# Kernel tuning notes

Hardware: AMD Instinct MI355X
Metric: run time of the kernel (lower is better)

Reference implementation:

```python
import jax, jax.numpy as jnp
import numpy as np
from jax.scipy.special import logsumexp

B, N, D = 8, 2048, 256
X_SLIDE, Y_SLIDE = 0.05, 0.05
ITERS = 20  # self.sinkhorn_iterations


def setup_inputs() -> dict:
    key = jax.random.key(0)
    k1, k2 = jax.random.split(key)
    return {
        "node_features": jax.random.normal(k1, (B, D, N), dtype=jnp.float32),
        "node_positions": jax.random.uniform(k2, (B, N, 2), dtype=jnp.float32),
        "active_nodes": jnp.ones((B, N), dtype=bool),
        "alpha": jnp.ones((1,), dtype=jnp.float32),  # bin_score parameter
    }


def log_sinkhorn_iterations(Z, log_mu, log_nu, iters):
    """Log-space Sinkhorn. Z: (b, M, K); log_mu: (b, M); log_nu: (b, K)."""
    u0 = jnp.zeros_like(log_mu)
    v0 = jnp.zeros_like(log_nu)

    def body(carry, _):
        u, v = carry
        u = log_mu - logsumexp(Z + v[:, None, :], axis=2)
        v = log_nu - logsumexp(Z + u[:, :, None], axis=1)
        return (u, v), None

    (u, v), _ = jax.lax.scan(body, (u0, v0), None, length=iters)
    return Z + u[:, :, None] + v[:, None, :]


def log_optimal_transport(scores, alpha, iters):
    """scores: (b, m, n); alpha: scalar bin score."""
    b, m, n = scores.shape
    dt = scores.dtype
    ms = jnp.asarray(m, dt)
    ns = jnp.asarray(n, dt)
    bins0 = jnp.broadcast_to(alpha, (b, m, 1))
    bins1 = jnp.broadcast_to(alpha, (b, 1, n))
    corner = jnp.broadcast_to(alpha, (b, 1, 1))
    couplings = jnp.concatenate(
        [jnp.concatenate([scores, bins0], axis=2),
         jnp.concatenate([bins1, corner], axis=2)], axis=1)  # (b, m+1, n+1)
    norm = -jnp.log(ms + ns)
    log_mu = jnp.concatenate([jnp.broadcast_to(norm, (m,)), (jnp.log(ns) + norm)[None]])
    log_nu = jnp.concatenate([jnp.broadcast_to(norm, (n,)), (jnp.log(ms) + norm)[None]])
    log_mu = jnp.broadcast_to(log_mu[None], (b, m + 1))
    log_nu = jnp.broadcast_to(log_nu[None], (b, n + 1))
    Z = log_sinkhorn_iterations(couplings, log_mu, log_nu, iters)
    return Z - norm


def spatial_cost(positions, x_slide, y_slide):
    """positions: (N, 2) -> bool (N, N) adjacency; diagonal excluded via 1e6 fill."""
    y = positions[:, 0]
    x = positions[:, 1]
    yd = jnp.abs(y[:, None] - y[None, :])
    xd = jnp.abs(x[:, None] - x[None, :])
    eye = jnp.eye(positions.shape[0], dtype=bool)
    yd = jnp.where(eye, 1e6, yd)
    xd = jnp.where(eye, 1e6, xd)
    return (xd <= x_slide * 2.0) & (yd <= y_slide * 2.0)


def reference(node_features, node_positions, active_nodes, alpha):
    # all nodes active -> indexing by active_nodes is identity, vectorize over batch
    a = alpha.reshape(())
    d = node_features.shape[1]
    scale = jnp.asarray(d, node_features.dtype) ** 0.5
    scores = jnp.einsum('bdn,bdm->bnm', node_features, node_features) / scale  # (B, N, N)
    n = scores.shape[-1]
    eye = jnp.eye(n, dtype=bool)
    scores = jnp.where(eye[None], -jnp.inf, scores)  # fill_diagonal_(-inf)
    Z = log_optimal_transport(scores, a, ITERS)  # (B, N+1, N+1)
    S = jnp.exp(Z)
    cost = jax.vmap(lambda p: spatial_cost(p, X_SLIDE, Y_SLIDE))(node_positions)
    S = S.at[:, :-1, :-1].multiply(cost.astype(S.dtype))
    return S
```

## Files before the change

kernel.cpp:

```cpp
#include <hip/hip_runtime.h>
#include <math.h>

#define BN    8
#define NN    2048
#define NP1   2049
#define VSTR  2056
#define DD    256
#define NITER 20
#define NBLK  256
#define GRP   32

typedef float f32x2 __attribute__((ext_vector_type(2)));
typedef float f32x4_t __attribute__((ext_vector_type(4)));
typedef short short8 __attribute__((ext_vector_type(8)));


__global__ void init_kernel(float* __restrict__ bvec, int nb, float* __restrict__ sums,
                            int* __restrict__ bar) {
    int tid = blockIdx.x * blockDim.x + threadIdx.x;
    int stride = gridDim.x * blockDim.x;
    for (int i = tid; i < nb; i += stride) bvec[i] = 1.0f;
    for (int i = tid; i < 41 * BN; i += stride) sums[i] = (i < BN) ? (float)NN : 0.0f;
    if (tid < BN * GRP) bar[tid] = 0;
}

__device__ __forceinline__ unsigned short f2bf(float f) {
    unsigned u = __builtin_bit_cast(unsigned, f);
    return (unsigned short)((u + 0x7fffu + ((u >> 16) & 1u)) >> 16);
}

__global__ __launch_bounds__(256) void f_to_bf16(const float* __restrict__ F,
                                                 unsigned char* __restrict__ F16) {
    int x0 = blockIdx.x * 64, k0 = blockIdx.y * 64, bb = blockIdx.z;
    __shared__ unsigned short tile[64][68];
    int t = threadIdx.x;
    const float* Fb = F + (size_t)bb * DD * NN;
#pragma unroll
    for (int q = 0; q < 16; q++) {
        int idx = q * 256 + t;
        int kk = idx >> 6, xx = idx & 63;
        tile[xx][kk] = f2bf(Fb[(size_t)(k0 + kk) * NN + x0 + xx]);
    }
    __syncthreads();
    int r = t >> 2, c = t & 3;
    const unsigned long long* src = (const unsigned long long*)&tile[r][c * 16];
    unsigned long long v0 = src[0], v1 = src[1], v2 = src[2], v3 = src[3];
    unsigned char* dst = F16 + (((size_t)bb * NN + x0 + r) * DD + k0) * 2 + c * 32;
    ((unsigned long long*)dst)[0] = v0;
    ((unsigned long long*)dst)[1] = v1;
    ((unsigned long long*)dst)[2] = v2;
    ((unsigned long long*)dst)[3] = v3;
}

__global__ __launch_bounds__(256) void build_k3(const unsigned char* __restrict__ F16,
                                                unsigned char* __restrict__ K8) {
    int idx = blockIdx.x, ti = 0;
    while (idx >= 16 - ti) { idx -= 16 - ti; ti++; }
    int tj = ti + idx;
    int bb = blockIdx.z;
    int i0 = ti * 128, j0 = tj * 128;
    const unsigned char* F16b = F16 + (size_t)bb * NN * DD * 2;

    __shared__ __align__(16) unsigned char Smem[128 * 80 * 2];
    unsigned char* Ab = Smem;
    unsigned char* Bb = Smem + 128 * 80;
    unsigned char* Cm = Smem;

    int t = threadIdx.x;
    int w = t >> 6, l = t & 63;
    int wr = w >> 1, wc = w & 1;
    int g = l >> 4, c16 = l & 15;

    f32x4_t acc[4][4];
#pragma unroll
    for (int r = 0; r < 4; r++)
#pragma unroll
        for (int c = 0; c < 4; c++) acc[r][c] = (f32x4_t){0.f, 0.f, 0.f, 0.f};

    int xr = t >> 2, q4 = t & 3;
    uint4 va0 = *(const uint4*)(F16b + ((size_t)(i0 + xr) * DD) * 2 + q4 * 16);
    uint4 va1 = *(const uint4*)(F16b + ((size_t)(i0 + 64 + xr) * DD) * 2 + q4 * 16);
    uint4 vb0 = *(const uint4*)(F16b + ((size_t)(j0 + xr) * DD) * 2 + q4 * 16);
    uint4 vb1 = *(const uint4*)(F16b + ((size_t)(j0 + 64 + xr) * DD) * 2 + q4 * 16);

    for (int k0 = 0; k0 < DD; k0 += 32) {
        *(uint4*)(Ab + xr * 80 + q4 * 16)        = va0;
        *(uint4*)(Ab + (64 + xr) * 80 + q4 * 16) = va1;
        *(uint4*)(Bb + xr * 80 + q4 * 16)        = vb0;
        *(uint4*)(Bb + (64 + xr) * 80 + q4 * 16) = vb1;
        __syncthreads();

        if (k0 + 32 < DD) {
            int kn = (k0 + 32) * 2;
            va0 = *(const uint4*)(F16b + (size_t)(i0 + xr) * DD * 2 + kn + q4 * 16);
            va1 = *(const uint4*)(F16b + (size_t)(i0 + 64 + xr) * DD * 2 + kn + q4 * 16);
            vb0 = *(const uint4*)(F16b + (size_t)(j0 + xr) * DD * 2 + kn + q4 * 16);
            vb1 = *(const uint4*)(F16b + (size_t)(j0 + 64 + xr) * DD * 2 + kn + q4 * 16);
        }

        short8 af[4], bf_[4];
#pragma unroll
        for (int rf = 0; rf < 4; rf++)
            af[rf] = *(const short8*)(Ab + (wr * 64 + rf * 16 + c16) * 80 + g * 16);
#pragma unroll
        for (int cf = 0; cf < 4; cf++)
            bf_[cf] = *(const short8*)(Bb + (wc * 64 + cf * 16 + c16) * 80 + g * 16);
#pragma unroll
        for (int rf = 0; rf < 4; rf++)
#pragma unroll
            for (int cf = 0; cf < 4; cf++)
                acc[rf][cf] = __builtin_amdgcn_mfma_f32_16x16x32_bf16(
                    af[rf], bf_[cf], acc[rf][cf], 0, 0, 0);
        __syncthreads();
    }

#pragma unroll
    for (int rf = 0; rf < 4; rf++) {
#pragma unroll
        for (int cf = 0; cf < 4; cf++) {
            int ib = wr * 64 + rf * 16 + g * 4;
            int jl = wc * 64 + cf * 16 + c16;
            float v[4];
#pragma unroll
            for (int r = 0; r < 4; r++) {
                float e = __expf(acc[rf][cf][r] * 0.0625f);
                if (i0 + ib + r == j0 + jl) e = 0.0f;
                v[r] = e;
            }
            unsigned wd = __builtin_amdgcn_cvt_pk_fp8_f32(v[0], v[1], 0, false);
            wd = __builtin_amdgcn_cvt_pk_fp8_f32(v[2], v[3], wd, true);
            *(unsigned*)(Cm + jl * 132 + ib) = wd;
        }
    }
    __syncthreads();

    unsigned char* K8b = K8 + (size_t)bb * NN * NN;
    int il = t >> 1, hh = t & 1;
    {
        unsigned wrow[16];
#pragma unroll
        for (int cq = 0; cq < 16; cq++) {
            int cb = hh * 64 + cq * 4;
            unsigned b0 = Cm[(cb + 0) * 132 + il];
            unsigned b1 = Cm[(cb + 1) * 132 + il];
            unsigned b2 = Cm[(cb + 2) * 132 + il];
            unsigned b3 = Cm[(cb + 3) * 132 + il];
            wrow[cq] = b0 | (b1 << 8) | (b2 << 16) | (b3 << 24);
        }
        uint4* dst = (uint4*)(K8b + (size_t)(i0 + il) * NN + j0 + hh * 64);
#pragma unroll
        for (int qq = 0; qq < 4; qq++) {
            uint4 u; u.x = wrow[qq * 4]; u.y = wrow[qq * 4 + 1];
            u.z = wrow[qq * 4 + 2]; u.w = wrow[qq * 4 + 3];
            dst[qq] = u;
        }
    }
    if (tj > ti) {
        const uint4* srcp = (const uint4*)(Cm + il * 132 + hh * 64);
        uint4 u0 = srcp[0], u1 = srcp[1], u2 = srcp[2], u3 = srcp[3];
        uint4* dst = (uint4*)(K8b + (size_t)(j0 + il) * NN + i0 + hh * 64);
        dst[0] = u0; dst[1] = u1; dst[2] = u2; dst[3] = u3;
    }
}

__global__ __launch_bounds__(256) void build_k_f32(const float* __restrict__ F,
                                                   float* __restrict__ out) {
    int ti = blockIdx.x, tj = blockIdx.y, bb = blockIdx.z;
    if (tj < ti) return;
    __shared__ float As[32][64];
    __shared__ float Bs[32][64];
    int t  = threadIdx.x;
    int tx = t & 15, ty = t >> 4;
    float acc[4][4] = {};
    const float* Fb = F + (size_t)bb * DD * NN;
    int i0 = ti * 64, j0 = tj * 64;
    for (int k0 = 0; k0 < DD; k0 += 32) {
#pragma unroll
        for (int v = 0; v < 2; v++) {
            int f = t + 256 * v;
            int row = f >> 4, c4 = (f & 15) * 4;
            *(float4*)&As[row][c4] = *(const float4*)&Fb[(size_t)(k0 + row) * NN + i0 + c4];
            *(float4*)&Bs[row][c4] = *(const float4*)&Fb[(size_t)(k0 + row) * NN + j0 + c4];
        }
        __syncthreads();
#pragma unroll
        for (int k = 0; k < 32; k++) {
            float4 av = *(float4*)&As[k][ty * 4];
            float4 bv = *(float4*)&Bs[k][tx * 4];
            float ar[4] = {av.x, av.y, av.z, av.w};
            float br[4] = {bv.x, bv.y, bv.z, bv.w};
#pragma unroll
            for (int r = 0; r < 4; r++)
#pragma unroll
                for (int c = 0; c < 4; c++)
                    acc[r][c] = fmaf(ar[r], br[c], acc[r][c]);
        }
        __syncthreads();
    }
#pragma unroll
    for (int r = 0; r < 4; r++) {
        int i = i0 + ty * 4 + r;
#pragma unroll
        for (int c = 0; c < 4; c++) {
            int j = j0 + tx * 4 + c;
            float Kv = (i == j) ? 0.0f : __expf(acc[r][c] * 0.0625f);
            float* outb = out + (size_t)bb * NP1 * NP1;
            outb[(size_t)i * NP1 + j] = Kv;
            if (tj > ti) outb[(size_t)j * NP1 + i] = Kv;
        }
    }
}

__global__ __launch_bounds__(1024) void sink_persist(const unsigned char* __restrict__ K8,
                                                     float* __restrict__ avec,
                                                     float* __restrict__ bvec,
                                                     int* __restrict__ bar,
                                                     const float* __restrict__ alpha) {
    int blk   = blockIdx.x;
    int batch = blk & 7;
    int rb    = blk >> 3;
    int tid   = threadIdx.x;
    int seg   = tid & 15;
    int row   = tid >> 4;
    int grow  = rb * 64 + row;

    __shared__ __align__(16) unsigned char Ks[64 * 2048];
    __shared__ float xs[16 * 132];
    __shared__ float wsum[16];

    {
        const int4* gsrc = (const int4*)(K8 + ((size_t)batch * NN + (size_t)rb * 64) * NN);
#pragma unroll
        for (int q = 0; q < 8; q++) {
            int idx = q * 1024 + tid;
            int4 v = gsrc[idx];
            int g = idx * 16;
            int r_ = g >> 11, bir = g & 2047;
            *(int4*)&Ks[r_ * 2048 + (bir ^ (((bir >> 7) & 7) << 4))] = v;
        }
    }

    float* av = avec + (size_t)batch * VSTR;
    float* bv = bvec + (size_t)batch * VSTR;
    int*   gbar = bar + batch * GRP;
    float E    = __expf(alpha[0]);
    float binA = 0.f, binB = 1.0f;
    int   ep   = 0;
    const float4* xp4 = (const float4*)(xs + seg * 132);
    const int kbase = row * 2048;
    const int sb    = seg * 128;
    const int sx    = (seg & 7) << 4;

#define MAC16(KI, ACC)                                                          \
    {                                                                           \
        int4 kv = *(const int4*)&Ks[kbase + ((sb + (KI) * 16) ^ sx)];           \
        float4 xa = xp4[(KI) * 4 + 0], xb = xp4[(KI) * 4 + 1];                  \
        float4 xc = xp4[(KI) * 4 + 2], xd = xp4[(KI) * 4 + 3];                  \
        f32x2 p0 = __builtin_amdgcn_cvt_pk_f32_fp8(kv.x, false);                \
        f32x2 p1 = __builtin_amdgcn_cvt_pk_f32_fp8(kv.x, true);                 \
        f32x2 p2 = __builtin_amdgcn_cvt_pk_f32_fp8(kv.y, false);                \
        f32x2 p3 = __builtin_amdgcn_cvt_pk_f32_fp8(kv.y, true);                 \
        f32x2 p4 = __builtin_amdgcn_cvt_pk_f32_fp8(kv.z, false);                \
        f32x2 p5 = __builtin_amdgcn_cvt_pk_f32_fp8(kv.z, true);                 \
        f32x2 p6 = __builtin_amdgcn_cvt_pk_f32_fp8(kv.w, false);                \
        f32x2 p7 = __builtin_amdgcn_cvt_pk_f32_fp8(kv.w, true);                 \
        ACC = fmaf(p0.x, xa.x, ACC); ACC = fmaf(p0.y, xa.y, ACC);               \
        ACC = fmaf(p1.x, xa.z, ACC); ACC = fmaf(p1.y, xa.w, ACC);               \
        ACC = fmaf(p2.x, xb.x, ACC); ACC = fmaf(p2.y, xb.y, ACC);               \
        ACC = fmaf(p3.x, xb.z, ACC); ACC = fmaf(p3.y, xb.w, ACC);               \
        ACC = fmaf(p4.x, xc.x, ACC); ACC = fmaf(p4.y, xc.y, ACC);               \
        ACC = fmaf(p5.x, xc.z, ACC); ACC = fmaf(p5.y, xc.w, ACC);               \
        ACC = fmaf(p6.x, xd.x, ACC); ACC = fmaf(p6.y, xd.y, ACC);               \
        ACC = fmaf(p7.x, xd.z, ACC); ACC = fmaf(p7.y, xd.w, ACC);               \
    }

#define SINK_PASS(XIN, XOUT, BIN_IN, BIN_OUT, LAST)                             \
    {                                                                           \
        float sv;                                                               \
        {           \
            float v0 = __hip_atomic_load((XIN) + 2 * tid, __ATOMIC_RELAXED,     \
                                         __HIP_MEMORY_SCOPE_AGENT);             \
            float v1 = __hip_atomic_load((XIN) + 2 * tid + 1, __ATOMIC_RELAXED, \
                                         __HIP_MEMORY_SCOPE_AGENT);             \
            int j = tid * 2;                                                    \
            float* d = xs + ((j >> 7) * 132 + (j & 127));                       \
            d[0] = v0; d[1] = v1;                                               \
            sv = v0 + v1;                                                       \
        }                                                                       \
        sv += __shfl_xor(sv, 1);  sv += __shfl_xor(sv, 2);                      \
        sv += __shfl_xor(sv, 4);  sv += __shfl_xor(sv, 8);                      \
        sv += __shfl_xor(sv, 16); sv += __shfl_xor(sv, 32);                     \
        if ((tid & 63) == 0) wsum[tid >> 6] = sv;                               \
        __syncthreads();                                                        \
        float S_cur = 0.f;                                                      \
        _Pragma("unroll")                                                       \
        for (int w2 = 0; w2 < 16; w2++) S_cur += wsum[w2];                      \
        float dot0 = 0.f, dot1 = 0.f;                                           \
        MAC16(0, dot0) MAC16(1, dot1) MAC16(2, dot0) MAC16(3, dot1)             \
        MAC16(4, dot0) MAC16(5, dot1) MAC16(6, dot0) MAC16(7, dot1)             \
        float dot = dot0 + dot1;                                                \
        dot += __shfl_xor(dot, 1);                                              \
        dot += __shfl_xor(dot, 2);                                              \
        dot += __shfl_xor(dot, 4);                                              \
        dot += __shfl_xor(dot, 8);                                              \
        float val = (1.0f / 4096.0f) / (dot + E * (BIN_IN));                    \
        BIN_OUT = 0.5f / (E * (S_cur + (BIN_IN)));                              \
        if ((tid & 15) == 0)                                                    \
            __hip_atomic_store(&(XOUT)[grow], val, __ATOMIC_RELAXED,            \
                               __HIP_MEMORY_SCOPE_AGENT);                       \
        __syncthreads();         \
        if (!(LAST)) {                                                          \
            ep++;                                                               \
            if (tid == 0)                                                       \
                __hip_atomic_store(&gbar[rb], ep, __ATOMIC_RELAXED,             \
                                   __HIP_MEMORY_SCOPE_AGENT);                   \
            if (tid < GRP) {                                                    \
                while (__hip_atomic_load(&gbar[tid], __ATOMIC_RELAXED,          \
                                         __HIP_MEMORY_SCOPE_AGENT) < ep)        \
                    __builtin_amdgcn_s_sleep(1);                                \
            }                                                                   \
            __syncthreads();                                                    \
        }                                                                       \
    }

    for (int it2 = 0; it2 < NITER; it2++) {
        SINK_PASS(bv, av, binB, binA, false);
        SINK_PASS(av, bv, binA, binB, (it2 == NITER - 1));
    }
#undef SINK_PASS
#undef MAC16

    if (tid == 0) { av[NN] = binA; bv[NN] = binB; }
}

__global__ __launch_bounds__(256) void sink_pass_f32(const float* __restrict__ K,
                                                     const float* __restrict__ xin,
                                                     float* __restrict__ xout,
                                                     const float* __restrict__ sum_in,
                                                     float* __restrict__ sum_out,
                                                     const float* __restrict__ alpha) {
    int bb = blockIdx.y;
    int i0 = blockIdx.x * 16;
    __shared__ float xsl[NN];
    __shared__ float rowa[16];
    const float* xinb = xin + (size_t)bb * VSTR;
    int t = threadIdx.x;
    for (int j = t; j < NN; j += 256) xsl[j] = xinb[j];
    __syncthreads();
    float E  = __expf(alpha[0]);
    float xN = xinb[NN];
    int wave = t >> 6, lane = t & 63;
    const float* Kb = K + (size_t)bb * NP1 * NP1;
    for (int r = wave; r < 16; r += 4) {
        int i = i0 + r;
        const float* rowp = Kb + (size_t)i * NP1;
        float acc = 0.f;
        for (int j = lane; j < NN; j += 64) acc = fmaf(rowp[j], xsl[j], acc);
#pragma unroll
        for (int off = 32; off >= 1; off >>= 1) acc += __shfl_xor(acc, off);
        if (lane == 0) {
            float v = (1.0f / 4096.0f) / (acc + E * xN);
            xout[(size_t)bb * VSTR + i] = v;
            rowa[r] = v;
        }
    }
    __syncthreads();
    if (t == 0) {
        float s = 0.f;
#pragma unroll
        for (int r = 0; r < 16; r++) s += rowa[r];
        atomicAdd(sum_out + bb, s);
        if (blockIdx.x == 0) xout[(size_t)bb * VSTR + NN] = 0.5f / (E * (sum_in[bb] + xN));
    }
}

template <bool FP8>
__global__ __launch_bounds__(256) void final_kernel(float* __restrict__ out,
                                                    const unsigned char* __restrict__ K8,
                                                    const float* __restrict__ avec,
                                                    const float* __restrict__ bvec,
                                                    const float* __restrict__ pos,
                                                    const float* __restrict__ alpha) {
    int bb = blockIdx.y;
    int i0 = blockIdx.x * 16;
    __shared__ float as_[16], ys[16], xs2[16];
    int t = threadIdx.x;
    if (t < 16) {
        int i = i0 + t;
        as_[t] = (i < NP1) ? avec[(size_t)bb * VSTR + i] : 0.f;
        if (i < NN) {
            ys[t]  = pos[((size_t)bb * NN + i) * 2 + 0];
            xs2[t] = pos[((size_t)bb * NN + i) * 2 + 1];
        } else {
            ys[t] = 1e9f; xs2[t] = 1e9f;
        }
    }
    __syncthreads();
    float E = __expf(alpha[0]);
    float* outb = out + (size_t)bb * NP1 * NP1;
    const unsigned char* K8b = K8 + (size_t)bb * NN * NN;
    for (int j = t; j < NP1; j += 256) {
        float bj = bvec[(size_t)bb * VSTR + j];
        bool jin = (j < NN);
        float yj = 0.f, xj = 0.f;
        if (jin) {
            yj = pos[((size_t)bb * NN + j) * 2 + 0];
            xj = pos[((size_t)bb * NN + j) * 2 + 1];
        }
#pragma unroll 1
        for (int r = 0; r < 16; r++) {
            int i = i0 + r;
            if (i >= NP1) break;
            size_t idx = (size_t)i * NP1 + j;
            float v;
            if (i < NN && jin) {
                float Kv;
                if constexpr (FP8)
                    Kv = __builtin_amdgcn_cvt_f32_fp8((int)K8b[(size_t)i * NN + j], 0);
                else
                    Kv = outb[idx];
                bool c = (fabsf(ys[r] - yj) <= 0.1f) && (fabsf(xs2[r] - xj) <= 0.1f);
                v = c ? Kv * as_[r] * bj * 4096.0f : 0.0f;
            } else {
                v = E * as_[r] * bj * 4096.0f;
            }
            outb[idx] = v;
        }
    }
}

extern "C" void kernel_launch(void* const* d_in, const int* in_sizes, int n_in,
                              void* d_out, int out_size, void* d_ws, size_t ws_size,
                              hipStream_t stream) {
    const float* F     = (const float*)d_in[0];
    const float* pos   = (const float*)d_in[1];
    const float* alpha = (const float*)d_in[3];
    float* out = (float*)d_out;
    float* ws  = (float*)d_ws;

    float* avec = ws;
    float* bvec = ws + BN * VSTR;
    float* sums = ws + 2 * BN * VSTR;
    int*   bar  = (int*)(sums + 41 * BN);
    float* psum = (float*)(bar + BN * GRP);
    unsigned char* K8  = (unsigned char*)(psum + 2 * BN * GRP);
    unsigned char* F16 = K8 + (size_t)BN * NN * NN;

    size_t need = (size_t)(2 * BN * VSTR + 41 * BN + 3 * BN * GRP) * 4
                + (size_t)BN * NN * NN + (size_t)BN * NN * DD * 2;
    bool fp8 = (ws_size >= need);

    hipLaunchKernelGGL(init_kernel, dim3(64), dim3(256), 0, stream, bvec, BN * VSTR,
                       sums, bar);

    if (fp8) {
        hipLaunchKernelGGL(f_to_bf16, dim3(NN / 64, DD / 64, BN), dim3(256), 0, stream,
                           F, F16);
        hipLaunchKernelGGL(build_k3, dim3(136, 1, BN), dim3(256), 0, stream, F16, K8);
        hipLaunchKernelGGL(sink_persist, dim3(NBLK), dim3(1024), 0, stream,
                           K8, avec, bvec, bar, alpha);
        hipLaunchKernelGGL((final_kernel<true>), dim3((NP1 + 15) / 16, BN), dim3(256), 0,
                           stream, out, K8, avec, bvec, pos, alpha);
    } else {
        hipLaunchKernelGGL(build_k_f32, dim3(32, 32, BN), dim3(256), 0, stream, F, out);
        const float* xin = bvec;
        float* xout = avec;
        for (int p = 1; p <= 2 * NITER; p++) {
            hipLaunchKernelGGL(sink_pass_f32, dim3(NN / 16, BN), dim3(256), 0, stream,
                               out, xin, xout, sums + (p - 1) * BN, sums + p * BN, alpha);
            float* tmp = (float*)xin; xin = xout; xout = tmp;
        }
        hipLaunchKernelGGL((final_kernel<false>), dim3((NP1 + 15) / 16, BN), dim3(256), 0,
                           stream, out, K8, avec, bvec, pos, alpha);
    }
}
```

Before: 324.3 us.

## Fuse final output kernel into persistent Sinkhorn kernel using LDS-resident K

Removes the separate final kernel and writes the output from the persistent Sinkhorn kernel. It reuses the fp8 K tile already held in LDS, keeps the last row scalings and the positions in shared memory, and adds one more grid barrier so the final column scalings are complete before writing. This avoids re-reading K8 from global memory and one kernel launch. The cost is 16KB of extra LDS for positions, which may hurt occupancy, and the output writes now run on only 256 blocks.

Result: faster. 274.1 us (-15.5%).

```diff
diff --git a/kernel.cpp b/kernel.cpp
--- a/kernel.cpp
+++ b/kernel.cpp
@@ -215,7 +215,9 @@
                                                      float* __restrict__ avec,
                                                      float* __restrict__ bvec,
                                                      int* __restrict__ bar,
-                                                     const float* __restrict__ alpha) {
+                                                     const float* __restrict__ alpha,
+                                                     const float* __restrict__ pos,
+                                                     float* __restrict__ outp) {
     int blk   = blockIdx.x;
     int batch = blk & 7;
     int rb    = blk >> 3;
@@ -227,6 +229,8 @@
     __shared__ __align__(16) unsigned char Ks[64 * 2048];
     __shared__ float xs[16 * 132];
     __shared__ float wsum[16];
+    __shared__ float ava[64];
+    __shared__ float posy[NN], posx[NN];
 
     {
         const int4* gsrc = (const int4*)(K8 + ((size_t)batch * NN + (size_t)rb * 64) * NN);
@@ -238,6 +242,11 @@
             int r_ = g >> 11, bir = g & 2047;
             *(int4*)&Ks[r_ * 2048 + (bir ^ (((bir >> 7) & 7) << 4))] = v;
         }
+        const float2* pp2 = (const float2*)(pos + (size_t)batch * NN * 2);
+        float2 p0 = pp2[tid];
+        float2 p1 = pp2[tid + 1024];
+        posy[tid] = p0.x;        posx[tid] = p0.y;
+        posy[tid + 1024] = p1.x; posx[tid + 1024] = p1.y;
     }
 
     float* av = avec + (size_t)batch * VSTR;
@@ -274,7 +283,7 @@
         ACC = fmaf(p7.x, xd.z, ACC); ACC = fmaf(p7.y, xd.w, ACC);               \
     }
 
-#define SINK_PASS(XIN, XOUT, BIN_IN, BIN_OUT, LAST)                             \
+#define SINK_PASS(XIN, XOUT, BIN_IN, BIN_OUT, SAVEA, LAST)                      \
     {                                                                           \
         float sv;                                                               \
         {           \
@@ -305,9 +314,11 @@
         dot += __shfl_xor(dot, 8);                                              \
         float val = (1.0f / 4096.0f) / (dot + E * (BIN_IN));                    \
         BIN_OUT = 0.5f / (E * (S_cur + (BIN_IN)));                              \
-        if ((tid & 15) == 0)                                                    \
+        if ((tid & 15) == 0) {                                                  \
             __hip_atomic_store(&(XOUT)[grow], val, __ATOMIC_RELAXED,            \
                                __HIP_MEMORY_SCOPE_AGENT);                       \
+            if (SAVEA) ava[tid >> 4] = val;                                     \
+        }                                                                       \
         __syncthreads();         \
         if (!(LAST)) {                                                          \
             ep++;                                                               \
@@ -324,13 +335,61 @@
     }
 
     for (int it2 = 0; it2 < NITER; it2++) {
-        SINK_PASS(bv, av, binB, binA, false);
-        SINK_PASS(av, bv, binA, binB, (it2 == NITER - 1));
+        SINK_PASS(bv, av, binB, binA, (it2 == NITER - 1), false);
+        SINK_PASS(av, bv, binA, binB, false, (it2 == NITER - 1));
     }
 #undef SINK_PASS
 #undef MAC16
 
     if (tid == 0) { av[NN] = binA; bv[NN] = binB; }
+
+    ep++;
+    if (tid == 0)
+        __hip_atomic_store(&gbar[rb], ep, __ATOMIC_RELAXED, __HIP_MEMORY_SCOPE_AGENT);
+    if (tid < GRP) {
+        while (__hip_atomic_load(&gbar[tid], __ATOMIC_RELAXED,
+                                 __HIP_MEMORY_SCOPE_AGENT) < ep)
+            __builtin_amdgcn_s_sleep(1);
+    }
+    __syncthreads();
+    {
+        float v0 = __hip_atomic_load(bv + 2 * tid, __ATOMIC_RELAXED,
+                                     __HIP_MEMORY_SCOPE_AGENT);
+        float v1 = __hip_atomic_load(bv + 2 * tid + 1, __ATOMIC_RELAXED,
+                                     __HIP_MEMORY_SCOPE_AGENT);
+        int j = tid * 2;
+        float* d = xs + ((j >> 7) * 132 + (j & 127));
+        d[0] = v0; d[1] = v1;
+    }
+    __syncthreads();
+
+    float* outb = outp + (size_t)batch * NP1 * NP1;
+    int c0 = tid, c1 = tid + 1024;
+    int lo0 = c0 ^ (((c0 >> 7) & 7) << 4);
+    int lo1 = c1 ^ (((c1 >> 7) & 7) << 4);
+    float b0 = xs[(c0 >> 7) * 132 + (c0 & 127)];
+    float b1 = xs[(c1 >> 7) * 132 + (c1 & 127)];
+    float y0 = posy[c0], x0 = posx[c0];
+    float y1 = posy[c1], x1 = posx[c1];
+#pragma unroll 4
+    for (int r = 0; r < 64; r++) {
+        int gr = rb * 64 + r;
+        float ai = ava[r];
+        float yi = posy[gr], xi = posx[gr];
+        float K0 = __builtin_amdgcn_cvt_f32_fp8((int)Ks[r * 2048 + lo0], 0);
+        float K1 = __builtin_amdgcn_cvt_f32_fp8((int)Ks[r * 2048 + lo1], 0);
+        bool cc0 = (fabsf(yi - y0) <= 0.1f) && (fabsf(xi - x0) <= 0.1f);
+        bool cc1 = (fabsf(yi - y1) <= 0.1f) && (fabsf(xi - x1) <= 0.1f);
+        outb[(size_t)gr * NP1 + c0] = cc0 ? K0 * ai * b0 * 4096.0f : 0.0f;
+        outb[(size_t)gr * NP1 + c1] = cc1 ? K1 * ai * b1 * 4096.0f : 0.0f;
+    }
+    if (tid < 64)
+        outb[(size_t)(rb * 64 + tid) * NP1 + NN] = E * ava[tid] * binB * 4096.0f;
+    if (rb == 0) {
+        outb[(size_t)NN * NP1 + c0] = E * binA * b0 * 4096.0f;
+        outb[(size_t)NN * NP1 + c1] = E * binA * b1 * 4096.0f;
+        if (tid == 0) outb[(size_t)NN * NP1 + NN] = E * binA * binB * 4096.0f;
+    }
 }
 
 __global__ __launch_bounds__(256) void sink_pass_f32(const float* __restrict__ K,
@@ -374,13 +433,11 @@
     }
 }
 
-template <bool FP8>
-__global__ __launch_bounds__(256) void final_kernel(float* __restrict__ out,
-                                                    const unsigned char* __restrict__ K8,
-                                                    const float* __restrict__ avec,
-                                                    const float* __restrict__ bvec,
-                                                    const float* __restrict__ pos,
-                                                    const float* __restrict__ alpha) {
+__global__ __launch_bounds__(256) void final_f32(float* __restrict__ out,
+                                                 const float* __restrict__ avec,
+                                                 const float* __restrict__ bvec,
+                                                 const float* __restrict__ pos,
+                                                 const float* __restrict__ alpha) {
     int bb = blockIdx.y;
     int i0 = blockIdx.x * 16;
     __shared__ float as_[16], ys[16], xs2[16];
@@ -398,7 +455,6 @@
     __syncthreads();
     float E = __expf(alpha[0]);
     float* outb = out + (size_t)bb * NP1 * NP1;
-    const unsigned char* K8b = K8 + (size_t)bb * NN * NN;
     for (int j = t; j < NP1; j += 256) {
         float bj = bvec[(size_t)bb * VSTR + j];
         bool jin = (j < NN);
@@ -414,11 +470,7 @@
             size_t idx = (size_t)i * NP1 + j;
             float v;
             if (i < NN && jin) {
-                float Kv;
-                if constexpr (FP8)
-                    Kv = __builtin_amdgcn_cvt_f32_fp8((int)K8b[(size_t)i * NN + j], 0);
-                else
-                    Kv = outb[idx];
+                float Kv = outb[idx];
                 bool c = (fabsf(ys[r] - yj) <= 0.1f) && (fabsf(xs2[r] - xj) <= 0.1f);
                 v = c ? Kv * as_[r] * bj * 4096.0f : 0.0f;
             } else {
@@ -458,9 +510,7 @@
                            F, F16);
         hipLaunchKernelGGL(build_k3, dim3(136, 1, BN), dim3(256), 0, stream, F16, K8);
         hipLaunchKernelGGL(sink_persist, dim3(NBLK), dim3(1024), 0, stream,
-                           K8, avec, bvec, bar, alpha);
-        hipLaunchKernelGGL((final_kernel<true>), dim3((NP1 + 15) / 16, BN), dim3(256), 0,
-                           stream, out, K8, avec, bvec, pos, alpha);
+                           K8, avec, bvec, bar, alpha, pos, out);
     } else {
         hipLaunchKernelGGL(build_k_f32, dim3(32, 32, BN), dim3(256), 0, stream, F, out);
         const float* xin = bvec;
@@ -470,7 +520,7 @@
                                out, xin, xout, sums + (p - 1) * BN, sums + p * BN, alpha);
             float* tmp = (float*)xin; xin = xout; xout = tmp;
         }
-        hipLaunchKernelGGL((final_kernel<false>), dim3((NP1 + 15) / 16, BN), dim3(256), 0,
-                           stream, out, K8, avec, bvec, pos, alpha);
-    }
-}
+        hipLaunchKernelGGL(final_f32, dim3((NP1 + 15) / 16, BN), dim3(256), 0,
+                           stream, out, avec, bvec, pos, alpha);
+    }
+}
```
